# Performance work log

Hardware: AMD Instinct MI355X
Metric: run time of the kernel (lower is better)

The kernel has to match this reference:

```python
import jax, jax.numpy as jnp
import numpy as np

B, L, D = 8, 256, 256
HN = 8            # head_num
HS = D // HN      # head_size
NEG = jnp.float32(-2.0**32 + 1)


def _split_heads(x):
    # torch.cat(torch.split(x, HS, dim=2), dim=0): head-major -> [HN*B, L, HS]
    b, l, _ = x.shape
    return x.reshape(b, l, HN, HS).transpose(2, 0, 1, 3).reshape(HN * b, l, HS)


def _split_heads_tm(t):
    # [B, L, L, D] -> [HN*B, L, L, HS], head-major on axis 0
    b, l, _, _ = t.shape
    return t.reshape(b, l, l, HN, HS).transpose(3, 0, 1, 2, 4).reshape(HN * b, l, l, HS)


def setup_inputs() -> dict:
    key = jax.random.key(0)
    ks = jax.random.split(key, 12)
    inp = {
        "queries": jax.random.normal(ks[0], (B, L, D), jnp.float32),
        "keys": jax.random.normal(ks[1], (B, L, D), jnp.float32),
        "time_mask": jnp.zeros((B, L, L), jnp.bool_),
        "attn_mask": jnp.triu(jnp.ones((L, L), jnp.bool_), k=1),  # causal: mask future
        "time_matrix_K": jax.random.normal(ks[2], (B, L, L, D), jnp.float32) * 0.05,
        "time_matrix_V": jax.random.normal(ks[3], (B, L, L, D), jnp.float32) * 0.05,
        "abs_pos_K": jax.random.normal(ks[4], (B, L, D), jnp.float32),
        "abs_pos_V": jax.random.normal(ks[5], (B, L, D), jnp.float32),
        "Q_w": jax.random.normal(ks[6], (D, D), jnp.float32) / np.sqrt(D),
        "Q_b": jnp.zeros((D,), jnp.float32),
        "K_w": jax.random.normal(ks[7], (D, D), jnp.float32) / np.sqrt(D),
        "K_b": jnp.zeros((D,), jnp.float32),
        "V_w": jax.random.normal(ks[8], (D, D), jnp.float32) / np.sqrt(D),
        "V_b": jnp.zeros((D,), jnp.float32),
    }
    return inp


def reference(queries, keys, time_mask, attn_mask, time_matrix_K, time_matrix_V,
              abs_pos_K, abs_pos_V, Q_w, Q_b, K_w, K_b, V_w, V_b):
    Q = queries @ Q_w.T + Q_b
    K = keys @ K_w.T + K_b
    V = keys @ V_w.T + V_b

    Q_, K_, V_ = _split_heads(Q), _split_heads(K), _split_heads(V)          # [HN*B, L, HS]
    tK_, tV_ = _split_heads_tm(time_matrix_K), _split_heads_tm(time_matrix_V)  # [HN*B, L, L, HS]
    pK_, pV_ = _split_heads(abs_pos_K), _split_heads(abs_pos_V)

    attn = jnp.einsum('bid,bjd->bij', Q_, K_)
    attn += jnp.einsum('bid,bjd->bij', Q_, pK_)
    attn += jnp.einsum('blij,blj->bli', tK_, Q_)
    attn = attn / jnp.sqrt(jnp.float32(HS))

    # NOTE: original expands time_mask batch-major (repeat_interleave) while
    # attn is head-major; reproduced faithfully.
    tm = jnp.repeat(time_mask, HN, axis=0)                # [B*HN, L, L]
    am = jnp.broadcast_to(attn_mask[None], attn.shape)
    attn = jnp.where(tm | am, NEG, attn)
    attn = jax.nn.softmax(attn, axis=-1)

    out = attn @ V_
    out += attn @ pV_
    out += jnp.einsum('bij,bijh->bih', attn, tV_)         # [HN*B, L, HS]

    # torch.cat(torch.split(out, B, dim=0), dim=2)
    out = out.reshape(HN, B, L, HS).transpose(1, 2, 0, 3).reshape(B, L, D)
    return out
```

## Files before the change

kernel.cpp:

```cpp
#include <hip/hip_runtime.h>
#include <math.h>

#define Bq 8
#define Lq 256
#define Dq 256
#define HNq 8
#define HSq 32
#define PADq 260

typedef float f4 __attribute__((ext_vector_type(4)));

#define PROJ_ROWS 8

__global__ __launch_bounds__(256) void proj_kernel(
    const float* __restrict__ queries, const float* __restrict__ keys,
    const float* __restrict__ apK, const float* __restrict__ apV,
    const float* __restrict__ Qw, const float* __restrict__ Qb,
    const float* __restrict__ Kw, const float* __restrict__ Kb,
    const float* __restrict__ Vw, const float* __restrict__ Vb,
    float* __restrict__ Q, float* __restrict__ KpK, float* __restrict__ VpV)
{
    __shared__ float inq[PROJ_ROWS][Dq];
    __shared__ float ink[PROJ_ROWS][Dq];
    const int r0 = blockIdx.x * PROJ_ROWS;
    const int tid = threadIdx.x;

    for (int idx = tid; idx < PROJ_ROWS * Dq; idx += 256) {
        int r = idx >> 8, c = idx & 255;
        inq[r][c] = queries[(size_t)(r0 + r) * Dq + c];
        ink[r][c] = keys[(size_t)(r0 + r) * Dq + c];
    }
    __syncthreads();

    const int d = tid;
    float aq[PROJ_ROWS], ak[PROJ_ROWS], av[PROJ_ROWS];
#pragma unroll
    for (int r = 0; r < PROJ_ROWS; ++r) { aq[r] = 0.f; ak[r] = 0.f; av[r] = 0.f; }

    const float4* qwr = (const float4*)(Qw + (size_t)d * Dq);
    const float4* kwr = (const float4*)(Kw + (size_t)d * Dq);
    const float4* vwr = (const float4*)(Vw + (size_t)d * Dq);

    for (int k4 = 0; k4 < Dq / 4; ++k4) {
        float4 wq = qwr[k4], wk = kwr[k4], wv = vwr[k4];
        int k = k4 * 4;
#pragma unroll
        for (int r = 0; r < PROJ_ROWS; ++r) {
            float i0 = inq[r][k], i1 = inq[r][k + 1], i2 = inq[r][k + 2], i3 = inq[r][k + 3];
            aq[r] += i0 * wq.x + i1 * wq.y + i2 * wq.z + i3 * wq.w;
            float j0 = ink[r][k], j1 = ink[r][k + 1], j2 = ink[r][k + 2], j3 = ink[r][k + 3];
            ak[r] += j0 * wk.x + j1 * wk.y + j2 * wk.z + j3 * wk.w;
            av[r] += j0 * wv.x + j1 * wv.y + j2 * wv.z + j3 * wv.w;
        }
    }

    const float qb = Qb[d], kb = Kb[d], vb = Vb[d];
#pragma unroll
    for (int r = 0; r < PROJ_ROWS; ++r) {
        size_t o = (size_t)(r0 + r) * Dq + d;
        Q[o]   = (aq[r] + qb) * 0.17677669529663687f;
        KpK[o] = ak[r] + kb + apK[o];
        VpV[o] = av[r] + vb + apV[o];
    }
}

__global__ __launch_bounds__(256) void attn_kernel(
    const float* __restrict__ Q, const float* __restrict__ KpK,
    const float* __restrict__ VpV,
    const float* __restrict__ tmK, const float* __restrict__ tmV,
    float* __restrict__ out)
{
    const int x   = blockIdx.x;
    const int b   = blockIdx.y;
    const int tid = threadIdx.x;
    const int w    = tid >> 6;
    const int lane = tid & 63;
    const int h    = lane >> 3;
    const int l8   = lane & 7;
    const int c4   = h * HSq + l8 * 4;

    __shared__ float qs[Dq];
    __shared__ float sb[HNq * PADq];
    __shared__ float po[4][Dq];

    const size_t rowB = (size_t)b * Lq * Dq;

    for (int hf = 0; hf < 2; ++hf) {
        const int i = hf ? (Lq - 1 - x) : x;

        if (tid < 64)
            ((f4*)qs)[tid] = ((const f4*)(Q + rowB + (size_t)i * Dq))[tid];
        __syncthreads();
        const f4 q4 = *(const f4*)(qs + c4);

        const float* tkB = tmK + ((size_t)(b * Lq + i) * Lq) * Dq;
        const float* tvB = tmV + ((size_t)(b * Lq + i) * Lq) * Dq;

#pragma unroll 2
        for (int j = w; j <= i; j += 4) {
            f4 tk = __builtin_nontemporal_load((const f4*)(tkB + (size_t)j * Dq + c4));
            f4 kp = *(const f4*)(KpK + rowB + (size_t)j * Dq + c4);
            float s = q4[0] * (tk[0] + kp[0]) + q4[1] * (tk[1] + kp[1])
                    + q4[2] * (tk[2] + kp[2]) + q4[3] * (tk[3] + kp[3]);
            s += __shfl_xor(s, 1);
            s += __shfl_xor(s, 2);
            s += __shfl_xor(s, 4);
            if (l8 == 0) sb[h * PADq + j] = s;
        }
        __syncthreads();

        {
            const int hh = tid >> 5, jl = tid & 31;
            float vv[8];
            float m = -3.0e38f;
#pragma unroll
            for (int k = 0; k < 8; ++k) {
                int j = jl + 32 * k;
                vv[k] = (j <= i) ? sb[hh * PADq + j] : -3.0e38f;
                m = fmaxf(m, vv[k]);
            }
#pragma unroll
            for (int off = 16; off >= 1; off >>= 1) m = fmaxf(m, __shfl_xor(m, off));
            float sum = 0.f;
#pragma unroll
            for (int k = 0; k < 8; ++k) { vv[k] = __expf(vv[k] - m); sum += vv[k]; }
#pragma unroll
            for (int off = 16; off >= 1; off >>= 1) sum += __shfl_xor(sum, off);
            const float inv = 1.0f / sum;
#pragma unroll
            for (int k = 0; k < 8; ++k) sb[hh * PADq + jl + 32 * k] = vv[k] * inv;
        }
        __syncthreads();

        f4 acc = {0.f, 0.f, 0.f, 0.f};
#pragma unroll 2
        for (int j = w; j <= i; j += 4) {
            float p = sb[h * PADq + j];
            f4 tv = __builtin_nontemporal_load((const f4*)(tvB + (size_t)j * Dq + c4));
            f4 vp = *(const f4*)(VpV + rowB + (size_t)j * Dq + c4);
            acc += p * (tv + vp);
        }
        *(f4*)(po[w] + c4) = acc;
        __syncthreads();

        out[rowB + (size_t)i * Dq + tid] =
            po[0][tid] + po[1][tid] + po[2][tid] + po[3][tid];
        __syncthreads();
    }
}

extern "C" void kernel_launch(void* const* d_in, const int* in_sizes, int n_in,
                              void* d_out, int out_size, void* d_ws, size_t ws_size,
                              hipStream_t stream) {
    const float* queries = (const float*)d_in[0];
    const float* keys    = (const float*)d_in[1];
    const float* tmK = (const float*)d_in[4];
    const float* tmV = (const float*)d_in[5];
    const float* apK = (const float*)d_in[6];
    const float* apV = (const float*)d_in[7];
    const float* Qw  = (const float*)d_in[8];
    const float* Qb  = (const float*)d_in[9];
    const float* Kw  = (const float*)d_in[10];
    const float* Kb  = (const float*)d_in[11];
    const float* Vw  = (const float*)d_in[12];
    const float* Vb  = (const float*)d_in[13];
    float* out = (float*)d_out;

    const size_t n = (size_t)Bq * Lq * Dq;
    float* Q   = (float*)d_ws;
    float* KpK = Q + n;
    float* VpV = KpK + n;

    proj_kernel<<<dim3((Bq * Lq) / PROJ_ROWS), 256, 0, stream>>>(
        queries, keys, apK, apV, Qw, Qb, Kw, Kb, Vw, Vb, Q, KpK, VpV);

    attn_kernel<<<dim3(Lq / 2, Bq), 256, 0, stream>>>(
        Q, KpK, VpV, tmK, tmV, out);
}
```

Measured before the change: 174.1 us.

## Split attention along key dimension with partial softmax and combine kernel

Replaces the per-row attention kernel with a split-K (flash-decoding style) scheme. Each block handles 8 query rows over one of four key-range chunks, writing partial accumulators plus per-head max and sum, and a new combine kernel merges them with log-sum-exp rescaling. The goal is better load balance and more concurrent blocks for the bandwidth-bound streaming of the time matrices. In exchange it adds extra workspace traffic for the partials, an extra kernel launch, and chunks that fall entirely in the masked future region do no work.

```diff
diff --git a/kernel.cpp b/kernel.cpp
--- a/kernel.cpp
+++ b/kernel.cpp
@@ -6,7 +6,9 @@
 #define Dq 256
 #define HNq 8
 #define HSq 32
-#define PADq 260
+#define RCH 8
+#define NSPL 4
+#define WP 65
 
 typedef float f4 __attribute__((ext_vector_type(4)));
 
@@ -64,89 +66,132 @@
     }
 }
 
-__global__ __launch_bounds__(256) void attn_kernel(
+__global__ __launch_bounds__(256, 4) void attn_part(
     const float* __restrict__ Q, const float* __restrict__ KpK,
     const float* __restrict__ VpV,
     const float* __restrict__ tmK, const float* __restrict__ tmV,
-    float* __restrict__ out)
+    float* __restrict__ pacc, float* __restrict__ pm, float* __restrict__ pl)
 {
-    const int x   = blockIdx.x;
-    const int b   = blockIdx.y;
-    const int tid = threadIdx.x;
+    const int id = blockIdx.x;
+    const int s  = id >> 8;
+    const int t  = id & 255;
+    const int b  = t >> 5;
+    const int cx = t & 31;
+    const int c  = (s & 1) ? cx : 31 - cx;
+    const int W  = 2 * (c + 1);
+    const int jlo = s * W;
+
+    const int tid  = threadIdx.x;
     const int w    = tid >> 6;
     const int lane = tid & 63;
     const int h    = lane >> 3;
     const int l8   = lane & 7;
-    const int c4   = h * HSq + l8 * 4;
-
-    __shared__ float qs[Dq];
-    __shared__ float sb[HNq * PADq];
+    const int c4   = lane * 4;
+
+    __shared__ float qs[RCH][Dq];
+    __shared__ float sb[RCH][HNq * WP];
     __shared__ float po[4][Dq];
 
     const size_t rowB = (size_t)b * Lq * Dq;
-
-    for (int hf = 0; hf < 2; ++hf) {
-        const int i = hf ? (Lq - 1 - x) : x;
-
-        if (tid < 64)
-            ((f4*)qs)[tid] = ((const f4*)(Q + rowB + (size_t)i * Dq))[tid];
-        __syncthreads();
-        const f4 q4 = *(const f4*)(qs + c4);
-
+    const int i0 = c * RCH;
+
+    for (int idx = tid; idx < RCH * (Dq / 4); idx += 256) {
+        int r = idx >> 6, q4 = idx & 63;
+        ((f4*)qs[r])[q4] = *(const f4*)(Q + rowB + (size_t)(i0 + r) * Dq + q4 * 4);
+    }
+    __syncthreads();
+
+    for (int r = 0; r < RCH; ++r) {
+        const int i = i0 + r;
+        const int jend = min(jlo + W, i + 1);
+        const f4 q4 = *(const f4*)(qs[r] + c4);
         const float* tkB = tmK + ((size_t)(b * Lq + i) * Lq) * Dq;
-        const float* tvB = tmV + ((size_t)(b * Lq + i) * Lq) * Dq;
-
 #pragma unroll 2
-        for (int j = w; j <= i; j += 4) {
+        for (int j = jlo + w; j < jend; j += 4) {
             f4 tk = __builtin_nontemporal_load((const f4*)(tkB + (size_t)j * Dq + c4));
             f4 kp = *(const f4*)(KpK + rowB + (size_t)j * Dq + c4);
-            float s = q4[0] * (tk[0] + kp[0]) + q4[1] * (tk[1] + kp[1])
-                    + q4[2] * (tk[2] + kp[2]) + q4[3] * (tk[3] + kp[3]);
-            s += __shfl_xor(s, 1);
-            s += __shfl_xor(s, 2);
-            s += __shfl_xor(s, 4);
-            if (l8 == 0) sb[h * PADq + j] = s;
-        }
-        __syncthreads();
-
-        {
-            const int hh = tid >> 5, jl = tid & 31;
-            float vv[8];
-            float m = -3.0e38f;
-#pragma unroll
-            for (int k = 0; k < 8; ++k) {
-                int j = jl + 32 * k;
-                vv[k] = (j <= i) ? sb[hh * PADq + j] : -3.0e38f;
-                m = fmaxf(m, vv[k]);
-            }
-#pragma unroll
-            for (int off = 16; off >= 1; off >>= 1) m = fmaxf(m, __shfl_xor(m, off));
-            float sum = 0.f;
-#pragma unroll
-            for (int k = 0; k < 8; ++k) { vv[k] = __expf(vv[k] - m); sum += vv[k]; }
-#pragma unroll
-            for (int off = 16; off >= 1; off >>= 1) sum += __shfl_xor(sum, off);
-            const float inv = 1.0f / sum;
-#pragma unroll
-            for (int k = 0; k < 8; ++k) sb[hh * PADq + jl + 32 * k] = vv[k] * inv;
-        }
-        __syncthreads();
-
+            float sc = q4[0] * (tk[0] + kp[0]) + q4[1] * (tk[1] + kp[1])
+                     + q4[2] * (tk[2] + kp[2]) + q4[3] * (tk[3] + kp[3]);
+            sc += __shfl_xor(sc, 1);
+            sc += __shfl_xor(sc, 2);
+            sc += __shfl_xor(sc, 4);
+            if (l8 == 0) sb[r][h * WP + (j - jlo)] = sc;
+        }
+    }
+    __syncthreads();
+
+    {
+        const int r  = tid >> 5;
+        const int hh = (tid >> 2) & 7;
+        const int l4 = tid & 3;
+        const int i  = i0 + r;
+        const int Lr = min(jlo + W, i + 1) - jlo;
+        float* sr = &sb[r][hh * WP];
+        float m = -3.0e38f;
+        for (int jj = l4; jj < Lr; jj += 4) m = fmaxf(m, sr[jj]);
+        m = fmaxf(m, __shfl_xor(m, 1));
+        m = fmaxf(m, __shfl_xor(m, 2));
+        float l = 0.f;
+        for (int jj = l4; jj < Lr; jj += 4) {
+            float p = __expf(sr[jj] - m);
+            sr[jj] = p;
+            l += p;
+        }
+        l += __shfl_xor(l, 1);
+        l += __shfl_xor(l, 2);
+        if (l4 == 0) {
+            size_t o = ((size_t)s * (Bq * Lq) + (size_t)b * Lq + i) * HNq + hh;
+            pm[o] = m;
+            pl[o] = l;
+        }
+    }
+    __syncthreads();
+
+    for (int r = 0; r < RCH; ++r) {
+        const int i = i0 + r;
+        const int jend = min(jlo + W, i + 1);
+        const float* tvB = tmV + ((size_t)(b * Lq + i) * Lq) * Dq;
         f4 acc = {0.f, 0.f, 0.f, 0.f};
 #pragma unroll 2
-        for (int j = w; j <= i; j += 4) {
-            float p = sb[h * PADq + j];
+        for (int j = jlo + w; j < jend; j += 4) {
+            float p = sb[r][h * WP + (j - jlo)];
             f4 tv = __builtin_nontemporal_load((const f4*)(tvB + (size_t)j * Dq + c4));
             f4 vp = *(const f4*)(VpV + rowB + (size_t)j * Dq + c4);
             acc += p * (tv + vp);
         }
         *(f4*)(po[w] + c4) = acc;
         __syncthreads();
-
-        out[rowB + (size_t)i * Dq + tid] =
-            po[0][tid] + po[1][tid] + po[2][tid] + po[3][tid];
+        float v = po[0][tid] + po[1][tid] + po[2][tid] + po[3][tid];
+        pacc[((size_t)s * (Bq * Lq) + (size_t)b * Lq + i) * Dq + tid] = v;
         __syncthreads();
     }
+}
+
+__global__ __launch_bounds__(256) void attn_combine(
+    const float* __restrict__ pacc, const float* __restrict__ pm,
+    const float* __restrict__ pl, float* __restrict__ out)
+{
+    const int row = blockIdx.x;
+    const int d = threadIdx.x;
+    const int h = d >> 5;
+
+    float ms[NSPL], ls[NSPL];
+    float M = -3.0e38f;
+#pragma unroll
+    for (int s = 0; s < NSPL; ++s) {
+        size_t o = ((size_t)s * (Bq * Lq) + row) * HNq + h;
+        ms[s] = pm[o];
+        ls[s] = pl[o];
+        M = fmaxf(M, ms[s]);
+    }
+    float L = 0.f, num = 0.f;
+#pragma unroll
+    for (int s = 0; s < NSPL; ++s) {
+        float e = __expf(ms[s] - M);
+        L += ls[s] * e;
+        num += pacc[((size_t)s * (Bq * Lq) + row) * Dq + d] * e;
+    }
+    out[(size_t)row * Dq + d] = num / L;
 }
 
 extern "C" void kernel_launch(void* const* d_in, const int* in_sizes, int n_in,
@@ -167,13 +212,18 @@
     float* out = (float*)d_out;
 
     const size_t n = (size_t)Bq * Lq * Dq;
-    float* Q   = (float*)d_ws;
-    float* KpK = Q + n;
-    float* VpV = KpK + n;
+    float* Q    = (float*)d_ws;
+    float* KpK  = Q + n;
+    float* VpV  = KpK + n;
+    float* pacc = VpV + n;
+    float* pm   = pacc + (size_t)NSPL * Bq * Lq * Dq;
+    float* pl   = pm + (size_t)NSPL * Bq * Lq * HNq;
 
     proj_kernel<<<dim3((Bq * Lq) / PROJ_ROWS), 256, 0, stream>>>(
         queries, keys, apK, apV, Qw, Qb, Kw, Kb, Vw, Vb, Q, KpK, VpV);
 
-    attn_kernel<<<dim3(Lq / 2, Bq), 256, 0, stream>>>(
-        Q, KpK, VpV, tmK, tmV, out);
-}
+    attn_part<<<dim3(NSPL * 256), 256, 0, stream>>>(
+        Q, KpK, VpV, tmK, tmV, pacc, pm, pl);
+
+    attn_combine<<<dim3(Bq * Lq), 256, 0, stream>>>(pacc, pm, pl, out);
+}
```

After: 216.9 us. 24.5% more time.

## Process paired query rows concurrently in attention kernel, sharing KpK/VpV loads

Applied to the files above, without the earlier changes.

Each block now handles rows i and L-1-i at the same time instead of one after the other. The KpK and VpV loads are shared between both rows, and two independent time-matrix streams are in flight per iteration. The grid is flattened with batch in the low bits so neighbouring blocks cover different batches. This removes one round of barriers and redundant K/V reads and adds memory-level parallelism, at the cost of more registers and shared memory and a divergent inner branch.

```diff
diff --git a/kernel.cpp b/kernel.cpp
--- a/kernel.cpp
+++ b/kernel.cpp
@@ -70,83 +70,106 @@
     const float* __restrict__ tmK, const float* __restrict__ tmV,
     float* __restrict__ out)
 {
-    const int x   = blockIdx.x;
-    const int b   = blockIdx.y;
-    const int tid = threadIdx.x;
+    const int id  = blockIdx.x;
+    const int b   = id & 7;
+    const int x   = id >> 3;
+    const int i1  = x;
+    const int i2  = Lq - 1 - x;
+
+    const int tid  = threadIdx.x;
     const int w    = tid >> 6;
     const int lane = tid & 63;
     const int h    = lane >> 3;
     const int l8   = lane & 7;
-    const int c4   = h * HSq + l8 * 4;
-
-    __shared__ float qs[Dq];
-    __shared__ float sb[HNq * PADq];
-    __shared__ float po[4][Dq];
+    const int c4   = lane * 4;
+
+    __shared__ float qs[2][Dq];
+    __shared__ float sb[2][HNq * PADq];
+    __shared__ float po[2][4][Dq];
 
     const size_t rowB = (size_t)b * Lq * Dq;
 
-    for (int hf = 0; hf < 2; ++hf) {
-        const int i = hf ? (Lq - 1 - x) : x;
-
-        if (tid < 64)
-            ((f4*)qs)[tid] = ((const f4*)(Q + rowB + (size_t)i * Dq))[tid];
-        __syncthreads();
-        const f4 q4 = *(const f4*)(qs + c4);
-
-        const float* tkB = tmK + ((size_t)(b * Lq + i) * Lq) * Dq;
-        const float* tvB = tmV + ((size_t)(b * Lq + i) * Lq) * Dq;
-
-#pragma unroll 2
-        for (int j = w; j <= i; j += 4) {
-            f4 tk = __builtin_nontemporal_load((const f4*)(tkB + (size_t)j * Dq + c4));
-            f4 kp = *(const f4*)(KpK + rowB + (size_t)j * Dq + c4);
-            float s = q4[0] * (tk[0] + kp[0]) + q4[1] * (tk[1] + kp[1])
-                    + q4[2] * (tk[2] + kp[2]) + q4[3] * (tk[3] + kp[3]);
-            s += __shfl_xor(s, 1);
-            s += __shfl_xor(s, 2);
-            s += __shfl_xor(s, 4);
-            if (l8 == 0) sb[h * PADq + j] = s;
-        }
-        __syncthreads();
-
-        {
-            const int hh = tid >> 5, jl = tid & 31;
-            float vv[8];
-            float m = -3.0e38f;
-#pragma unroll
-            for (int k = 0; k < 8; ++k) {
-                int j = jl + 32 * k;
-                vv[k] = (j <= i) ? sb[hh * PADq + j] : -3.0e38f;
-                m = fmaxf(m, vv[k]);
-            }
-#pragma unroll
-            for (int off = 16; off >= 1; off >>= 1) m = fmaxf(m, __shfl_xor(m, off));
-            float sum = 0.f;
-#pragma unroll
-            for (int k = 0; k < 8; ++k) { vv[k] = __expf(vv[k] - m); sum += vv[k]; }
-#pragma unroll
-            for (int off = 16; off >= 1; off >>= 1) sum += __shfl_xor(sum, off);
-            const float inv = 1.0f / sum;
-#pragma unroll
-            for (int k = 0; k < 8; ++k) sb[hh * PADq + jl + 32 * k] = vv[k] * inv;
-        }
-        __syncthreads();
-
-        f4 acc = {0.f, 0.f, 0.f, 0.f};
-#pragma unroll 2
-        for (int j = w; j <= i; j += 4) {
-            float p = sb[h * PADq + j];
-            f4 tv = __builtin_nontemporal_load((const f4*)(tvB + (size_t)j * Dq + c4));
-            f4 vp = *(const f4*)(VpV + rowB + (size_t)j * Dq + c4);
-            acc += p * (tv + vp);
-        }
-        *(f4*)(po[w] + c4) = acc;
-        __syncthreads();
-
-        out[rowB + (size_t)i * Dq + tid] =
-            po[0][tid] + po[1][tid] + po[2][tid] + po[3][tid];
-        __syncthreads();
-    }
+    if (tid < 128) {
+        int r = tid >> 6, qi = tid & 63;
+        ((f4*)qs[r])[qi] =
+            *((const f4*)(Q + rowB + (size_t)(r ? i2 : i1) * Dq) + qi);
+    }
+    __syncthreads();
+    const f4 qa = *(const f4*)(qs[0] + c4);
+    const f4 qb4 = *(const f4*)(qs[1] + c4);
+
+    const float* tk1 = tmK + ((size_t)(b * Lq + i1) * Lq) * Dq;
+    const float* tk2 = tmK + ((size_t)(b * Lq + i2) * Lq) * Dq;
+    const float* tv1 = tmV + ((size_t)(b * Lq + i1) * Lq) * Dq;
+    const float* tv2 = tmV + ((size_t)(b * Lq + i2) * Lq) * Dq;
+
+    for (int j = w; j <= i2; j += 4) {
+        f4 kp = *(const f4*)(KpK + rowB + (size_t)j * Dq + c4);
+        f4 t2 = __builtin_nontemporal_load((const f4*)(tk2 + (size_t)j * Dq + c4));
+        float s2 = qb4[0] * (t2[0] + kp[0]) + qb4[1] * (t2[1] + kp[1])
+                 + qb4[2] * (t2[2] + kp[2]) + qb4[3] * (t2[3] + kp[3]);
+        s2 += __shfl_xor(s2, 1);
+        s2 += __shfl_xor(s2, 2);
+        s2 += __shfl_xor(s2, 4);
+        if (l8 == 0) sb[1][h * PADq + j] = s2;
+        if (j <= i1) {
+            f4 t1 = __builtin_nontemporal_load((const f4*)(tk1 + (size_t)j * Dq + c4));
+            float s1 = qa[0] * (t1[0] + kp[0]) + qa[1] * (t1[1] + kp[1])
+                     + qa[2] * (t1[2] + kp[2]) + qa[3] * (t1[3] + kp[3]);
+            s1 += __shfl_xor(s1, 1);
+            s1 += __shfl_xor(s1, 2);
+            s1 += __shfl_xor(s1, 4);
+            if (l8 == 0) sb[0][h * PADq + j] = s1;
+        }
+    }
+    __syncthreads();
+
+    {
+        const int r  = tid >> 7;
+        const int hh = (tid >> 4) & 7;
+        const int jl = tid & 15;
+        const int i  = r ? i2 : i1;
+        float* sr = &sb[r][hh * PADq];
+        float vv[16];
+        float m = -3.0e38f;
+#pragma unroll
+        for (int k = 0; k < 16; ++k) {
+            int j = jl + 16 * k;
+            vv[k] = (j <= i) ? sr[j] : -3.0e38f;
+            m = fmaxf(m, vv[k]);
+        }
+#pragma unroll
+        for (int off = 8; off >= 1; off >>= 1) m = fmaxf(m, __shfl_xor(m, off));
+        float sum = 0.f;
+#pragma unroll
+        for (int k = 0; k < 16; ++k) { vv[k] = __expf(vv[k] - m); sum += vv[k]; }
+#pragma unroll
+        for (int off = 8; off >= 1; off >>= 1) sum += __shfl_xor(sum, off);
+        const float inv = 1.0f / sum;
+#pragma unroll
+        for (int k = 0; k < 16; ++k) sr[jl + 16 * k] = vv[k] * inv;
+    }
+    __syncthreads();
+
+    f4 a1 = {0.f, 0.f, 0.f, 0.f};
+    f4 a2 = {0.f, 0.f, 0.f, 0.f};
+    for (int j = w; j <= i2; j += 4) {
+        f4 vp = *(const f4*)(VpV + rowB + (size_t)j * Dq + c4);
+        f4 t2 = __builtin_nontemporal_load((const f4*)(tv2 + (size_t)j * Dq + c4));
+        a2 += sb[1][h * PADq + j] * (t2 + vp);
+        if (j <= i1) {
+            f4 t1 = __builtin_nontemporal_load((const f4*)(tv1 + (size_t)j * Dq + c4));
+            a1 += sb[0][h * PADq + j] * (t1 + vp);
+        }
+    }
+    *(f4*)(po[0][w] + c4) = a1;
+    *(f4*)(po[1][w] + c4) = a2;
+    __syncthreads();
+
+    out[rowB + (size_t)i1 * Dq + tid] =
+        po[0][0][tid] + po[0][1][tid] + po[0][2][tid] + po[0][3][tid];
+    out[rowB + (size_t)i2 * Dq + tid] =
+        po[1][0][tid] + po[1][1][tid] + po[1][2][tid] + po[1][3][tid];
 }
 
 extern "C" void kernel_launch(void* const* d_in, const int* in_sizes, int n_in,
@@ -174,6 +197,6 @@
     proj_kernel<<<dim3((Bq * Lq) / PROJ_ROWS), 256, 0, stream>>>(
         queries, keys, apK, apV, Qw, Qb, Kw, Kb, Vw, Vb, Q, KpK, VpV);
 
-    attn_kernel<<<dim3(Lq / 2, Bq), 256, 0, stream>>>(
+    attn_kernel<<<dim3(Bq * Lq / 2), 256, 0, stream>>>(
         Q, KpK, VpV, tmK, tmV, out);
 }
```

Measured after the change: 165.7 us. 1.05x faster.

## Process eight query rows per block to reuse K/V loads and raise loads in flight

Applied to the files above, without the earlier changes.

The attention kernel now handles eight query rows per block (four from the front and four from the back for causal balance) instead of two rows in sequence. Each loaded KpK/VpV row is shared across all eight rows, and the eight independent time-matrix loads per iteration raise memory-level parallelism. Softmax normalisation moves to the output step, dividing by a stored row sum. The cost is a much larger shared-memory footprint (about 66 KB of sb) and more registers, which cuts occupancy, and the grid shrinks to 256 blocks.

```diff
diff --git a/kernel.cpp b/kernel.cpp
--- a/kernel.cpp
+++ b/kernel.cpp
@@ -70,81 +70,113 @@
     const float* __restrict__ tmK, const float* __restrict__ tmV,
     float* __restrict__ out)
 {
-    const int x   = blockIdx.x;
-    const int b   = blockIdx.y;
-    const int tid = threadIdx.x;
+    const int id = blockIdx.x;
+    const int b  = id & 7;
+    const int c  = id >> 3;
+
+    const int tid  = threadIdx.x;
     const int w    = tid >> 6;
     const int lane = tid & 63;
     const int h    = lane >> 3;
     const int l8   = lane & 7;
-    const int c4   = h * HSq + l8 * 4;
-
-    __shared__ float qs[Dq];
-    __shared__ float sb[HNq * PADq];
-    __shared__ float po[4][Dq];
+    const int c4   = lane * 4;
+
+    int R[8];
+#pragma unroll
+    for (int r = 0; r < 4; ++r) { R[r] = 4 * c + r; R[4 + r] = 252 - 4 * c + r; }
+    const int imax = R[7];
+
+    __shared__ float qs[8][Dq];
+    __shared__ float sb[8][HNq * PADq];
+    __shared__ float po[2][4][Dq];
+    __shared__ float ll[8][HNq];
 
     const size_t rowB = (size_t)b * Lq * Dq;
 
-    for (int hf = 0; hf < 2; ++hf) {
-        const int i = hf ? (Lq - 1 - x) : x;
-
-        if (tid < 64)
-            ((f4*)qs)[tid] = ((const f4*)(Q + rowB + (size_t)i * Dq))[tid];
+    for (int idx = tid; idx < 8 * 64; idx += 256) {
+        int r = idx >> 6, qi = idx & 63;
+        ((f4*)qs[r])[qi] = *((const f4*)(Q + rowB + (size_t)R[r] * Dq) + qi);
+    }
+    __syncthreads();
+
+    f4 qr[8];
+#pragma unroll
+    for (int r = 0; r < 8; ++r) qr[r] = *(const f4*)(qs[r] + c4);
+
+    const float* tkB[8];
+    const float* tvB[8];
+#pragma unroll
+    for (int r = 0; r < 8; ++r) {
+        tkB[r] = tmK + ((size_t)(b * Lq + R[r]) * Lq) * Dq;
+        tvB[r] = tmV + ((size_t)(b * Lq + R[r]) * Lq) * Dq;
+    }
+
+    for (int j = w; j <= imax; j += 4) {
+        f4 kp = *(const f4*)(KpK + rowB + (size_t)j * Dq + c4);
+#pragma unroll
+        for (int r = 0; r < 8; ++r) {
+            if (j <= R[r]) {
+                f4 tk = __builtin_nontemporal_load(
+                            (const f4*)(tkB[r] + (size_t)j * Dq + c4));
+                float s = qr[r][0] * (tk[0] + kp[0]) + qr[r][1] * (tk[1] + kp[1])
+                        + qr[r][2] * (tk[2] + kp[2]) + qr[r][3] * (tk[3] + kp[3]);
+                s += __shfl_xor(s, 1);
+                s += __shfl_xor(s, 2);
+                s += __shfl_xor(s, 4);
+                if (l8 == 0) sb[r][h * PADq + j] = s;
+            }
+        }
+    }
+    __syncthreads();
+
+    {
+        const int r  = tid >> 5;
+        const int hh = (tid >> 2) & 7;
+        const int l4 = tid & 3;
+        const int i  = (r < 4) ? (4 * c + r) : (248 - 4 * c + r);
+        float* sr = &sb[r][hh * PADq];
+        float m = -3.0e38f;
+        for (int jj = l4; jj <= i; jj += 4) m = fmaxf(m, sr[jj]);
+        m = fmaxf(m, __shfl_xor(m, 1));
+        m = fmaxf(m, __shfl_xor(m, 2));
+        float l = 0.f;
+        for (int jj = l4; jj <= i; jj += 4) {
+            float p = __expf(sr[jj] - m);
+            sr[jj] = p;
+            l += p;
+        }
+        l += __shfl_xor(l, 1);
+        l += __shfl_xor(l, 2);
+        if (l4 == 0) ll[r][hh] = l;
+    }
+    __syncthreads();
+
+    f4 acc[8];
+#pragma unroll
+    for (int r = 0; r < 8; ++r) acc[r] = (f4){0.f, 0.f, 0.f, 0.f};
+
+    for (int j = w; j <= imax; j += 4) {
+        f4 vp = *(const f4*)(VpV + rowB + (size_t)j * Dq + c4);
+#pragma unroll
+        for (int r = 0; r < 8; ++r) {
+            if (j <= R[r]) {
+                f4 tv = __builtin_nontemporal_load(
+                            (const f4*)(tvB[r] + (size_t)j * Dq + c4));
+                acc[r] += sb[r][h * PADq + j] * (tv + vp);
+            }
+        }
+    }
+
+#pragma unroll
+    for (int rp = 0; rp < 8; rp += 2) {
+        *(f4*)(po[0][w] + c4) = acc[rp];
+        *(f4*)(po[1][w] + c4) = acc[rp + 1];
         __syncthreads();
-        const f4 q4 = *(const f4*)(qs + c4);
-
-        const float* tkB = tmK + ((size_t)(b * Lq + i) * Lq) * Dq;
-        const float* tvB = tmV + ((size_t)(b * Lq + i) * Lq) * Dq;
-
-#pragma unroll 2
-        for (int j = w; j <= i; j += 4) {
-            f4 tk = __builtin_nontemporal_load((const f4*)(tkB + (size_t)j * Dq + c4));
-            f4 kp = *(const f4*)(KpK + rowB + (size_t)j * Dq + c4);
-            float s = q4[0] * (tk[0] + kp[0]) + q4[1] * (tk[1] + kp[1])
-                    + q4[2] * (tk[2] + kp[2]) + q4[3] * (tk[3] + kp[3]);
-            s += __shfl_xor(s, 1);
-            s += __shfl_xor(s, 2);
-            s += __shfl_xor(s, 4);
-            if (l8 == 0) sb[h * PADq + j] = s;
-        }
-        __syncthreads();
-
-        {
-            const int hh = tid >> 5, jl = tid & 31;
-            float vv[8];
-            float m = -3.0e38f;
-#pragma unroll
-            for (int k = 0; k < 8; ++k) {
-                int j = jl + 32 * k;
-                vv[k] = (j <= i) ? sb[hh * PADq + j] : -3.0e38f;
-                m = fmaxf(m, vv[k]);
-            }
-#pragma unroll
-            for (int off = 16; off >= 1; off >>= 1) m = fmaxf(m, __shfl_xor(m, off));
-            float sum = 0.f;
-#pragma unroll
-            for (int k = 0; k < 8; ++k) { vv[k] = __expf(vv[k] - m); sum += vv[k]; }
-#pragma unroll
-            for (int off = 16; off >= 1; off >>= 1) sum += __shfl_xor(sum, off);
-            const float inv = 1.0f / sum;
-#pragma unroll
-            for (int k = 0; k < 8; ++k) sb[hh * PADq + jl + 32 * k] = vv[k] * inv;
-        }
-        __syncthreads();
-
-        f4 acc = {0.f, 0.f, 0.f, 0.f};
-#pragma unroll 2
-        for (int j = w; j <= i; j += 4) {
-            float p = sb[h * PADq + j];
-            f4 tv = __builtin_nontemporal_load((const f4*)(tvB + (size_t)j * Dq + c4));
-            f4 vp = *(const f4*)(VpV + rowB + (size_t)j * Dq + c4);
-            acc += p * (tv + vp);
-        }
-        *(f4*)(po[w] + c4) = acc;
-        __syncthreads();
-
-        out[rowB + (size_t)i * Dq + tid] =
-            po[0][tid] + po[1][tid] + po[2][tid] + po[3][tid];
+        const int hh = tid >> 5;
+        float o0 = po[0][0][tid] + po[0][1][tid] + po[0][2][tid] + po[0][3][tid];
+        float o1 = po[1][0][tid] + po[1][1][tid] + po[1][2][tid] + po[1][3][tid];
+        out[rowB + (size_t)R[rp] * Dq + tid]     = o0 / ll[rp][hh];
+        out[rowB + (size_t)R[rp + 1] * Dq + tid] = o1 / ll[rp + 1][hh];
         __syncthreads();
     }
 }
@@ -174,6 +206,6 @@
     proj_kernel<<<dim3((Bq * Lq) / PROJ_ROWS), 256, 0, stream>>>(
         queries, keys, apK, apV, Qw, Qb, Kw, Kb, Vw, Vb, Q, KpK, VpV);
 
-    attn_kernel<<<dim3(Lq / 2, Bq), 256, 0, stream>>>(
+    attn_kernel<<<dim3(Bq * Lq / 8), 256, 0, stream>>>(
         Q, KpK, VpV, tmK, tmV, out);
 }
```

Result: slower. 353.4 us (+103.0%).
